# Performance work log

Measured on AMD Instinct MI355X. Metric: run time of the kernel, lower is better.

The kernel has to match this reference:

```python
import jax, jax.numpy as jnp
import numpy as np

B, S, H = 4, 2048, 896
NH, NKV, HD = 14, 2, 64
ROPE_THETA = 1e6


def setup_inputs() -> dict:
    key = jax.random.key(0)
    ks = jax.random.split(key, 8)
    s = 0.02
    return {
        "hidden_states": jax.random.normal(ks[0], (B, S, H), jnp.float32),
        "position_ids": jnp.arange(S, dtype=jnp.int64 if jax.config.jax_enable_x64 else jnp.int32)[None, :],
        "Wq": jax.random.normal(ks[1], (NH * HD, H), jnp.float32) * s,
        "bq": jax.random.normal(ks[2], (NH * HD,), jnp.float32) * s,
        "Wk": jax.random.normal(ks[3], (NKV * HD, H), jnp.float32) * s,
        "bk": jax.random.normal(ks[4], (NKV * HD,), jnp.float32) * s,
        "Wv": jax.random.normal(ks[5], (NKV * HD, H), jnp.float32) * s,
        "bv": jax.random.normal(ks[6], (NKV * HD,), jnp.float32) * s,
        "Wo": jax.random.normal(ks[7], (H, NH * HD), jnp.float32) * s,
    }


def _rope_cos_sin(position_ids, dtype):
    # inv_freq: [HD/2]
    inv_freq = 1.0 / (ROPE_THETA ** (jnp.arange(0, HD, 2, dtype=jnp.float32) / HD))
    # freqs: [1, S, HD/2]
    freqs = position_ids.astype(jnp.float32)[:, :, None] * inv_freq[None, None, :]
    emb = jnp.concatenate([freqs, freqs], axis=-1)  # [1, S, HD]
    return jnp.cos(emb).astype(dtype), jnp.sin(emb).astype(dtype)


def _rotate_half(x):
    x1, x2 = x[..., : HD // 2], x[..., HD // 2 :]
    return jnp.concatenate([-x2, x1], axis=-1)


def reference(hidden_states, position_ids, Wq, bq, Wk, bk, Wv, bv, Wo):
    bsz, q_len, _ = hidden_states.shape
    q = hidden_states @ Wq.T + bq  # [B,S,NH*HD]
    k = hidden_states @ Wk.T + bk  # [B,S,NKV*HD]
    v = hidden_states @ Wv.T + bv
    q = q.reshape(bsz, q_len, NH, HD).transpose(0, 2, 1, 3)    # [B,NH,S,HD]
    k = k.reshape(bsz, q_len, NKV, HD).transpose(0, 2, 1, 3)   # [B,NKV,S,HD]
    v = v.reshape(bsz, q_len, NKV, HD).transpose(0, 2, 1, 3)

    cos, sin = _rope_cos_sin(position_ids, hidden_states.dtype)
    cos, sin = cos[:, None, :, :], sin[:, None, :, :]  # broadcast over heads
    q = q * cos + _rotate_half(q) * sin
    k = k * cos + _rotate_half(k) * sin

    # GQA: repeat kv heads to NH
    n_rep = NH // NKV
    k = jnp.repeat(k, n_rep, axis=1)  # [B,NH,S,HD]
    v = jnp.repeat(v, n_rep, axis=1)

    scale = 1.0 / jnp.sqrt(jnp.asarray(HD, hidden_states.dtype))
    scores = jnp.einsum("bhqd,bhkd->bhqk", q, k) * scale  # [B,NH,S,S]
    causal = jnp.tril(jnp.ones((q_len, q_len), dtype=bool))
    scores = jnp.where(causal[None, None], scores, jnp.finfo(scores.dtype).min)
    probs = jax.nn.softmax(scores, axis=-1)
    attn = jnp.einsum("bhqk,bhkd->bhqd", probs, v)  # [B,NH,S,HD]
    attn = attn.transpose(0, 2, 1, 3).reshape(bsz, q_len, NH * HD)
    return attn @ Wo.T
```

## Files before the change

kernel.cpp:

```cpp
#include <hip/hip_runtime.h>
#include <stdint.h>

#define SB    2048
#define HID   896
#define NHEADS 14
#define NKVH  2
#define HDIM  64
#define BATCH 4
#define MROWS (BATCH*SB)
#define KVW   (NKVH*HDIM)
#define PANEL (SB*HDIM)

typedef short bfrag __attribute__((ext_vector_type(8)));
typedef float f32x4 __attribute__((ext_vector_type(4)));

__device__ __forceinline__ float b2f(unsigned short u) {
    unsigned int x = ((unsigned int)u) << 16;
    float f;
    __builtin_memcpy(&f, &x, 4);
    return f;
}
__device__ __forceinline__ unsigned short f2b(float f) {
    unsigned int x;
    __builtin_memcpy(&x, &f, 4);
    x += 0x7fffu + ((x >> 16) & 1u);
    return (unsigned short)(x >> 16);
}
__device__ __forceinline__ unsigned int pack_bf16(float lo, float hi) {
    unsigned int a, b;
    __builtin_memcpy(&a, &lo, 4);
    __builtin_memcpy(&b, &hi, 4);
    return __builtin_amdgcn_perm(b, a, 0x07060302);
}

__device__ __forceinline__ void async16(void* lds, const void* g) {
    __builtin_amdgcn_global_load_lds(
        (const __attribute__((address_space(1))) unsigned int*)g,
        (__attribute__((address_space(3))) unsigned int*)lds, 16, 0, 0);
}

#define N_HS  (MROWS*HID)
#define N_WQ  (HID*HID)
#define N_BQ  (HID)
#define N_WK  (KVW*HID)
#define N_BK  (KVW)
#define N_WO  (HID*HID)
#define C0 ((size_t)N_HS)
#define C1 (C0 + N_WQ)
#define C2 (C1 + N_BQ)
#define C3 (C2 + N_WK)
#define C4 (C3 + N_BK)
#define C5 (C4 + N_WK)
#define C6 (C5 + N_BK)
#define C7 (C6 + N_WO)

__global__ __launch_bounds__(256) void cvt_kernel(
    const float* __restrict__ a0, const float* __restrict__ a1,
    const float* __restrict__ a2, const float* __restrict__ a3,
    const float* __restrict__ a4, const float* __restrict__ a5,
    const float* __restrict__ a6, const float* __restrict__ a7,
    unsigned short* __restrict__ d0, unsigned short* __restrict__ d1,
    unsigned short* __restrict__ d2, unsigned short* __restrict__ d3,
    unsigned short* __restrict__ d4, unsigned short* __restrict__ d5,
    unsigned short* __restrict__ d6, unsigned short* __restrict__ d7)
{
    size_t i = ((size_t)blockIdx.x * 256 + threadIdx.x) * 4;
    if (i >= C7) return;
    const float* s; unsigned short* d; size_t off;
    if      (i < C0) { s = a0; d = d0; off = i; }
    else if (i < C1) { s = a1; d = d1; off = i - C0; }
    else if (i < C2) { s = a2; d = d2; off = i - C1; }
    else if (i < C3) { s = a3; d = d3; off = i - C2; }
    else if (i < C4) { s = a4; d = d4; off = i - C3; }
    else if (i < C5) { s = a5; d = d5; off = i - C4; }
    else if (i < C6) { s = a6; d = d6; off = i - C5; }
    else             { s = a7; d = d7; off = i - C6; }
    float4 v = *(const float4*)(s + off);
    ushort4 o;
    o.x = f2b(v.x); o.y = f2b(v.y); o.z = f2b(v.z); o.w = f2b(v.w);
    *(ushort4*)(d + off) = o;
}

template<int EPI>
__device__ __forceinline__ void gemm128(
    unsigned short* __restrict__ Al, unsigned short* __restrict__ Bl,
    const unsigned short* __restrict__ A, int lda,
    const unsigned short* __restrict__ W, int ldw,
    const unsigned short* __restrict__ bias,
    void* __restrict__ Cv, int ldc, int m0, int n0, int K,
    unsigned short* __restrict__ VT)
{
    const int tid  = threadIdx.x;
    const int wave = tid >> 6;
    const int lane = tid & 63;
    const int col  = lane & 15;
    const int quad = lane >> 4;
    const int wm   = (wave >> 1) * 64;
    const int wn   = (wave & 1) * 64;
    const int srow = lane >> 2;
    const int scol = (lane & 3) * 8;

    f32x4 acc[4][4] = {};

    auto stage = [&](int buf, int k0) {
#pragma unroll
        for (int i = 0; i < 2; ++i) {
            const int c = wave*2 + i;
            async16(Al + buf*4096 + c*512,
                    A + (size_t)(m0 + c*16 + srow)*lda + k0 + scol);
            async16(Bl + buf*4096 + c*512,
                    W + (size_t)(n0 + c*16 + srow)*ldw + k0 + scol);
        }
    };

    stage(0, 0);
    if (K > 32) stage(1, 32);
    int t = 0;
    for (int k0 = 0; k0 < K; k0 += 32, ++t) {
        const bool more1 = (k0 + 32 < K);
        const bool more2 = (k0 + 64 < K);
        if (more2) stage((t + 2) % 3, k0 + 64);
        if (more2)      asm volatile("s_waitcnt vmcnt(8)" ::: "memory");
        else if (more1) asm volatile("s_waitcnt vmcnt(4)" ::: "memory");
        else            asm volatile("s_waitcnt vmcnt(0)" ::: "memory");
        asm volatile("s_barrier" ::: "memory");
        const unsigned short* Ab = Al + (t % 3)*4096;
        const unsigned short* Bb = Bl + (t % 3)*4096;
        bfrag a[4], b[4];
#pragma unroll
        for (int mb = 0; mb < 4; ++mb)
            a[mb] = *(const bfrag*)(Ab + (wm + mb*16 + col)*32 + quad*8);
#pragma unroll
        for (int nb = 0; nb < 4; ++nb)
            b[nb] = *(const bfrag*)(Bb + (wn + nb*16 + col)*32 + quad*8);
#pragma unroll
        for (int mb = 0; mb < 4; ++mb)
#pragma unroll
            for (int nb = 0; nb < 4; ++nb)
                acc[mb][nb] = __builtin_amdgcn_mfma_f32_16x16x32_bf16(
                    a[mb], b[nb], acc[mb][nb], 0, 0, 0);
        asm volatile("s_barrier" ::: "memory");
    }

    if (EPI == 2) {
#pragma unroll
        for (int nb = 0; nb < 4; ++nb) {
            const int n = wn + nb*16 + col;
            const float bv = b2f(bias[n]);
            const int kvh = n >> 6;
#pragma unroll
            for (int mb = 0; mb < 4; ++mb) {
                const int m = m0 + wm + mb*16 + quad*4;
                const int bb = m >> 11, s = m & (SB-1);
                const int cc = (s >> 5) & 1;
                const int qv = (s >> 3) & 3;
                const int jb = s & 7;
                ushort4 w;
                w.x = f2b(acc[mb][nb][0] + bv);
                w.y = f2b(acc[mb][nb][1] + bv);
                w.z = f2b(acc[mb][nb][2] + bv);
                w.w = f2b(acc[mb][nb][3] + bv);
                *(ushort4*)(VT + (size_t)(bb*NKVH + kvh)*PANEL
                            + (size_t)((s >> 6)*8 + cc*4 + nb)*512
                            + (qv*16 + col)*8 + jb) = w;
            }
        }
    } else {
#pragma unroll
        for (int nb = 0; nb < 4; ++nb) {
            const int n = n0 + wn + nb*16 + col;
            const float bv = bias ? b2f(bias[n]) : 0.0f;
#pragma unroll
            for (int mb = 0; mb < 4; ++mb) {
                const size_t base = (size_t)(m0 + wm + mb*16 + quad*4) * ldc + n;
#pragma unroll
                for (int r = 0; r < 4; ++r) {
                    const float v = acc[mb][nb][r] + bv;
                    if (EPI == 1) ((float*)Cv)[base + (size_t)r * ldc] = v;
                    else ((unsigned short*)Cv)[base + (size_t)r * ldc] = f2b(v);
                }
            }
        }
    }
}

__global__ __launch_bounds__(256) void qkv_gemm(
    const unsigned short* __restrict__ hs,
    const unsigned short* __restrict__ Wq, const unsigned short* __restrict__ bq,
    const unsigned short* __restrict__ Wk, const unsigned short* __restrict__ bk,
    const unsigned short* __restrict__ Wv, const unsigned short* __restrict__ bv,
    unsigned short* __restrict__ Qw, unsigned short* __restrict__ Kw,
    unsigned short* __restrict__ Vp)
{
    __shared__ __align__(16) unsigned short Al[3][128*32];
    __shared__ __align__(16) unsigned short Bl[3][128*32];
    const int m0  = blockIdx.x * 128;
    const int seg = blockIdx.y;
    if (seg < 7)
        gemm128<0>(&Al[0][0], &Bl[0][0], hs, HID, Wq, HID, bq, Qw, HID, m0, seg*128, HID, nullptr);
    else if (seg == 7)
        gemm128<0>(&Al[0][0], &Bl[0][0], hs, HID, Wk, HID, bk, Kw, KVW, m0, 0, HID, nullptr);
    else
        gemm128<2>(&Al[0][0], &Bl[0][0], hs, HID, Wv, HID, bv, nullptr, 0, m0, 0, HID, Vp);
}

__global__ __launch_bounds__(256) void out_gemm(
    const unsigned short* __restrict__ Aw, const unsigned short* __restrict__ Wo,
    float* __restrict__ out)
{
    __shared__ __align__(16) unsigned short Al[3][128*32];
    __shared__ __align__(16) unsigned short Bl[3][128*32];
    gemm128<1>(&Al[0][0], &Bl[0][0], Aw, HID, Wo, HID, nullptr, out, HID,
               blockIdx.x * 128, blockIdx.y * 128, HID, nullptr);
}

__global__ __launch_bounds__(256) void trig_kernel(float2* __restrict__ tab)
{
    const int i = blockIdx.x * 256 + threadIdx.x;
    const int pos = i >> 5, pair = i & 31;
    const float inv = exp2f(-(float)(2*pair) * (19.9315685693f / 64.0f));
    float s, c;
    sincosf((float)pos * inv, &s, &c);
    tab[i] = make_float2(c, s);
}

__global__ __launch_bounds__(256) void rope_kernel(unsigned short* __restrict__ Q,
                                                   const unsigned short* __restrict__ Kw,
                                                   unsigned short* __restrict__ Kp,
                                                   const float2* __restrict__ tab)
{
    const int idx  = blockIdx.x * 256 + threadIdx.x;
    const int pair = idx & 31;
    const int head = (idx >> 5) & 15;
    const int m    = idx >> 9;
    const int pos  = m & (SB - 1);
    const float2 cs = tab[pos*32 + pair];
    const float c = cs.x, s = cs.y;
    if (head < NHEADS) {
        const float mul = 0.1803368801111f;
        unsigned short* base = Q + (size_t)m * HID + (size_t)head * HDIM;
        const float x1 = b2f(base[pair]);
        const float x2 = b2f(base[pair + 32]);
        base[pair]      = f2b((x1 * c - x2 * s) * mul);
        base[pair + 32] = f2b((x2 * c + x1 * s) * mul);
    } else {
        const int kvh = head - NHEADS;
        const unsigned short* src = Kw + (size_t)m * KVW + (size_t)kvh * HDIM;
        const float x1 = b2f(src[pair]);
        const float x2 = b2f(src[pair + 32]);
        const float y1 = x1 * c - x2 * s;
        const float y2 = x2 * c + x1 * s;
        const int bb = m >> 11, sq = m & (SB - 1);
        const int tile = sq >> 6, r6 = sq & 63;
        const int kb = r6 >> 4, colk = r6 & 15;
        const int quad = pair >> 3, j = pair & 7;
        unsigned short* panel = Kp + (size_t)(bb*NKVH + kvh) * PANEL;
        const size_t off0 = (size_t)(tile*8 + kb*2)*512 + (quad*16 + colk)*8 + j;
        panel[off0]       = f2b(y1);
        panel[off0 + 512] = f2b(y2);
    }
}

__global__ __launch_bounds__(64, 2) void flash_kernel(
    const unsigned short* __restrict__ Q,
    const unsigned short* __restrict__ Kp,
    const unsigned short* __restrict__ Vp,
    unsigned short* __restrict__ Aw)
{
    const int bid  = blockIdx.x;
    const int cidx = bid / 56;
    const int hb   = bid - cidx * 56;
    const int h    = hb % NHEADS;
    const int b    = hb / NHEADS;
    const int kvh  = h / 7;
    const int chunk = 63 - cidx;

    const int lane = threadIdx.x;
    const int col  = lane & 15;
    const int quad = lane >> 4;

    const int idxA = (col + ((quad & 1) << 5)) << 2;
    const int idxB = idxA + 64;
    const bool hi  = (quad >= 2);

    const unsigned short* Qb  = Q  + (size_t)b * SB * HID + (size_t)h * HDIM;
    const unsigned short* Kpp = Kp + (size_t)(b*NKVH + kvh) * PANEL;
    const unsigned short* Vpp = Vp + (size_t)(b*NKVH + kvh) * PANEL;

    bfrag ones;
#pragma unroll
    for (int jj = 0; jj < 8; ++jj) ones[jj] = (short)0x3F80;

    const int qrow  = chunk * 32;
    const int nsteps = (chunk >> 1) + 1;

    bfrag qf[2][2];
#pragma unroll
    for (int qb = 0; qb < 2; ++qb) {
        const unsigned short* qr = Qb + (size_t)(qrow + qb*16 + col) * HID;
        qf[qb][0] = *(const bfrag*)(qr + quad*8);
        qf[qb][1] = *(const bfrag*)(qr + 32 + quad*8);
    }

    f32x4 o[2][4] = {};
    f32x4 lac[2] = {};

    f32x4 scur[2][4];
    {
        bfrag kc0[4][2];
#pragma unroll
        for (int kb = 0; kb < 4; ++kb) {
            kc0[kb][0] = *(const bfrag*)(Kpp + (size_t)(kb*2 + 0)*512 + lane*8);
            kc0[kb][1] = *(const bfrag*)(Kpp + (size_t)(kb*2 + 1)*512 + lane*8);
        }
#pragma unroll
        for (int kb = 0; kb < 4; ++kb)
#pragma unroll
            for (int qb = 0; qb < 2; ++qb) {
                f32x4 z = {};
                z = __builtin_amdgcn_mfma_f32_16x16x32_bf16(kc0[kb][0], qf[qb][0], z, 0, 0, 0);
                z = __builtin_amdgcn_mfma_f32_16x16x32_bf16(kc0[kb][1], qf[qb][1], z, 0, 0, 0);
                scur[qb][kb] = z;
            }
    }

    for (int step = 0; step < nsteps; ++step) {
        const size_t T = (size_t)step * 4096;
        const bool more = (step + 1 < nsteps);

        bfrag vf[2][4];
#pragma unroll
        for (int cc = 0; cc < 2; ++cc)
#pragma unroll
            for (int nb = 0; nb < 4; ++nb)
                vf[cc][nb] = *(const bfrag*)(Vpp + T + (cc*4 + nb)*512 + lane*8);
        bfrag kn[4][2];
        if (more) {
#pragma unroll
            for (int kb = 0; kb < 4; ++kb) {
                kn[kb][0] = *(const bfrag*)(Kpp + T + 4096 + (kb*2+0)*512 + lane*8);
                kn[kb][1] = *(const bfrag*)(Kpp + T + 4096 + (kb*2+1)*512 + lane*8);
            }
        }

        const int k0 = step * 64;
        unsigned int pk[2][4][2];
#pragma unroll
        for (int qb = 0; qb < 2; ++qb) {
            float pv[4][4];
#pragma unroll
            for (int kb = 0; kb < 4; ++kb)
#pragma unroll
                for (int r = 0; r < 4; ++r)
                    pv[kb][r] = __builtin_amdgcn_exp2f(scur[qb][kb][r]);
            if (step == nsteps - 1) {
                const int q = qrow + qb*16 + col;
#pragma unroll
                for (int kb = 0; kb < 4; ++kb)
#pragma unroll
                    for (int r = 0; r < 4; ++r)
                        if (k0 + kb*16 + quad*4 + r > q) pv[kb][r] = 0.f;
            }
#pragma unroll
            for (int kb = 0; kb < 4; ++kb) {
                pk[qb][kb][0] = pack_bf16(pv[kb][0], pv[kb][1]);
                pk[qb][kb][1] = pack_bf16(pv[kb][2], pv[kb][3]);
            }
        }

#pragma unroll
        for (int cc = 0; cc < 2; ++cc)
#pragma unroll
            for (int qb = 0; qb < 2; ++qb) {
                unsigned int D[4];
#pragma unroll
                for (int jj = 0; jj < 4; ++jj) {
                    const int idx = (jj < 2) ? idxA : idxB;
                    const int t0 = __builtin_amdgcn_ds_bpermute(idx, (int)pk[qb][2*cc][jj & 1]);
                    const int t1 = __builtin_amdgcn_ds_bpermute(idx, (int)pk[qb][2*cc+1][jj & 1]);
                    D[jj] = (unsigned int)(hi ? t1 : t0);
                }
                bfrag pf;
                __builtin_memcpy(&pf, D, 16);
                lac[qb] = __builtin_amdgcn_mfma_f32_16x16x32_bf16(ones, pf, lac[qb], 0, 0, 0);
#pragma unroll
                for (int nb = 0; nb < 4; ++nb)
                    o[qb][nb] = __builtin_amdgcn_mfma_f32_16x16x32_bf16(
                        vf[cc][nb], pf, o[qb][nb], 0, 0, 0);
            }

        if (more) {
            f32x4 snext[2][4];
#pragma unroll
            for (int kb = 0; kb < 4; ++kb)
#pragma unroll
                for (int qb = 0; qb < 2; ++qb) {
                    f32x4 z = {};
                    z = __builtin_amdgcn_mfma_f32_16x16x32_bf16(kn[kb][0], qf[qb][0], z, 0, 0, 0);
                    z = __builtin_amdgcn_mfma_f32_16x16x32_bf16(kn[kb][1], qf[qb][1], z, 0, 0, 0);
                    snext[qb][kb] = z;
                }
#pragma unroll
            for (int qb = 0; qb < 2; ++qb)
#pragma unroll
                for (int kb = 0; kb < 4; ++kb)
                    scur[qb][kb] = snext[qb][kb];
        }
    }

#pragma unroll
    for (int qb = 0; qb < 2; ++qb) {
        const float inv = 1.0f / lac[qb][0];
        const size_t row = (size_t)b * SB + qrow + qb*16 + col;
#pragma unroll
        for (int nb = 0; nb < 4; ++nb) {
            ushort4 w;
            w.x = f2b(o[qb][nb][0] * inv);
            w.y = f2b(o[qb][nb][1] * inv);
            w.z = f2b(o[qb][nb][2] * inv);
            w.w = f2b(o[qb][nb][3] * inv);
            *(ushort4*)(Aw + row * HID + h*HDIM + nb*16 + quad*4) = w;
        }
    }
}

extern "C" void kernel_launch(void* const* d_in, const int* in_sizes, int n_in,
                              void* d_out, int out_size, void* d_ws, size_t ws_size,
                              hipStream_t stream)
{
    (void)in_sizes; (void)n_in; (void)out_size; (void)ws_size;
    const float* hs_f = (const float*)d_in[0];
    const float* Wq_f = (const float*)d_in[2];
    const float* bq_f = (const float*)d_in[3];
    const float* Wk_f = (const float*)d_in[4];
    const float* bk_f = (const float*)d_in[5];
    const float* Wv_f = (const float*)d_in[6];
    const float* bv_f = (const float*)d_in[7];
    const float* Wo_f = (const float*)d_in[8];
    float* out = (float*)d_out;

    char* ws = (char*)d_ws;
    float2* tab = (float2*)ws;
    ws += ((size_t)SB * 32 * sizeof(float2) + 255) & ~(size_t)255;
    auto take = [&](size_t elems) {
        unsigned short* p = (unsigned short*)ws;
        ws += ((elems * 2 + 255) & ~(size_t)255);
        return p;
    };
    unsigned short* hs = take(N_HS);
    unsigned short* Wq = take(N_WQ);
    unsigned short* bq = take(N_BQ);
    unsigned short* Wk = take(N_WK);
    unsigned short* bk = take(N_BK);
    unsigned short* Wv = take(N_WK);
    unsigned short* bv = take(N_BK);
    unsigned short* Wo = take(N_WO);
    unsigned short* Qw = take((size_t)MROWS * HID);
    unsigned short* Kw = take((size_t)MROWS * KVW);
    unsigned short* Kp = take((size_t)MROWS * KVW);
    unsigned short* Vp = take((size_t)MROWS * KVW);
    unsigned short* Aw = take((size_t)MROWS * HID);

    trig_kernel<<<dim3(SB*32/256), 256, 0, stream>>>(tab);
    cvt_kernel<<<dim3((C7/4 + 255)/256), 256, 0, stream>>>(
        hs_f, Wq_f, bq_f, Wk_f, bk_f, Wv_f, bv_f, Wo_f,
        hs, Wq, bq, Wk, bk, Wv, bv, Wo);
    qkv_gemm<<<dim3(MROWS/128, 9), 256, 0, stream>>>(hs, Wq, bq, Wk, bk, Wv, bv,
                                                     Qw, Kw, Vp);
    rope_kernel<<<dim3((MROWS*16*32)/256), 256, 0, stream>>>(Qw, Kw, Kp, tab);
    flash_kernel<<<dim3(64*NHEADS*BATCH), 64, 0, stream>>>(Qw, Kp, Vp, Aw);
    out_gemm<<<dim3(MROWS/128, HID/128), 256, 0, stream>>>(Aw, Wo, out);
}
```

Baseline: 197.8 us.

## Fuse RoPE into QKV GEMM epilogue and merge trig table into convert kernel

Applies rotary embedding and the Q scale directly in the QKV GEMM epilogue, pairing accumulator blocks nb and nb+2 so each wave holds both halves of a head. K is rotated and written straight into the flash panel layout, which removes the separate rope kernel and the Kw intermediate buffer round trip. The cos/sin table is now built by extra blocks appended to the convert kernel, saving a launch. The cost is scattered table loads and uncoalesced 2-byte stores in the epilogue.

```diff
diff --git a/kernel.cpp b/kernel.cpp
--- a/kernel.cpp
+++ b/kernel.cpp
@@ -10,6 +10,7 @@
 #define MROWS (BATCH*SB)
 #define KVW   (NKVH*HDIM)
 #define PANEL (SB*HDIM)
+#define QSC   0.1803368801111f
 
 typedef short bfrag __attribute__((ext_vector_type(8)));
 typedef float f32x4 __attribute__((ext_vector_type(4)));
@@ -53,6 +54,7 @@
 #define C5 (C4 + N_WK)
 #define C6 (C5 + N_BK)
 #define C7 (C6 + N_WO)
+#define NB_CVT ((C7/4 + 255)/256)
 
 __global__ __launch_bounds__(256) void cvt_kernel(
     const float* __restrict__ a0, const float* __restrict__ a1,
@@ -62,8 +64,18 @@
     unsigned short* __restrict__ d0, unsigned short* __restrict__ d1,
     unsigned short* __restrict__ d2, unsigned short* __restrict__ d3,
     unsigned short* __restrict__ d4, unsigned short* __restrict__ d5,
-    unsigned short* __restrict__ d6, unsigned short* __restrict__ d7)
-{
+    unsigned short* __restrict__ d6, unsigned short* __restrict__ d7,
+    float2* __restrict__ tab)
+{
+    if (blockIdx.x >= NB_CVT) {
+        const int i = (blockIdx.x - (int)NB_CVT) * 256 + threadIdx.x;
+        const int pos = i >> 5, pair = i & 31;
+        const float inv = exp2f(-(float)(2*pair) * (19.9315685693f / 64.0f));
+        float s, c;
+        sincosf((float)pos * inv, &s, &c);
+        tab[i] = make_float2(c, s);
+        return;
+    }
     size_t i = ((size_t)blockIdx.x * 256 + threadIdx.x) * 4;
     if (i >= C7) return;
     const float* s; unsigned short* d; size_t off;
@@ -88,7 +100,7 @@
     const unsigned short* __restrict__ W, int ldw,
     const unsigned short* __restrict__ bias,
     void* __restrict__ Cv, int ldc, int m0, int n0, int K,
-    unsigned short* __restrict__ VT)
+    unsigned short* __restrict__ VT, const float2* __restrict__ tab)
 {
     const int tid  = threadIdx.x;
     const int wave = tid >> 6;
@@ -165,6 +177,59 @@
                             + (qv*16 + col)*8 + jb) = w;
             }
         }
+    } else if (EPI == 3) {
+#pragma unroll
+        for (int nb = 0; nb < 2; ++nb) {
+            const int n  = n0 + wn + nb*16 + col;
+            const float bv0 = b2f(bias[n]);
+            const float bv2 = b2f(bias[n + 32]);
+            const int pair = nb*16 + col;
+#pragma unroll
+            for (int mb = 0; mb < 4; ++mb) {
+                const int row = m0 + wm + mb*16 + quad*4;
+                const size_t base = (size_t)row * ldc;
+#pragma unroll
+                for (int r = 0; r < 4; ++r) {
+                    const int pos = (row + r) & (SB-1);
+                    const float2 cs = tab[pos*32 + pair];
+                    const float xl = acc[mb][nb][r]   + bv0;
+                    const float xh = acc[mb][nb+2][r] + bv2;
+                    ((unsigned short*)Cv)[base + (size_t)r*ldc + n]
+                        = f2b((xl*cs.x - xh*cs.y) * QSC);
+                    ((unsigned short*)Cv)[base + (size_t)r*ldc + n + 32]
+                        = f2b((xh*cs.x + xl*cs.y) * QSC);
+                }
+            }
+        }
+    } else if (EPI == 4) {
+#pragma unroll
+        for (int nb = 0; nb < 2; ++nb) {
+            const int n   = wn + nb*16 + col;
+            const int kvh = n >> 6;
+            const int pair = n & 63;
+            const float bv0 = b2f(bias[n]);
+            const float bv2 = b2f(bias[n + 32]);
+            const int dq = pair >> 3, j = pair & 7;
+#pragma unroll
+            for (int mb = 0; mb < 4; ++mb) {
+                const int m = m0 + wm + mb*16 + quad*4;
+                const int bb = m >> 11;
+                unsigned short* pan = VT + (size_t)(bb*NKVH + kvh)*PANEL;
+#pragma unroll
+                for (int r = 0; r < 4; ++r) {
+                    const int s = (m + r) & (SB-1);
+                    const float2 cs = tab[s*32 + pair];
+                    const float xl = acc[mb][nb][r]   + bv0;
+                    const float xh = acc[mb][nb+2][r] + bv2;
+                    const int tile = s >> 6, sk = s & 63;
+                    const int kb = sk >> 4, colk = sk & 15;
+                    const size_t off = (size_t)(tile*8 + kb*2)*512
+                                     + (dq*16 + colk)*8 + j;
+                    pan[off]       = f2b(xl*cs.x - xh*cs.y);
+                    pan[off + 512] = f2b(xh*cs.x + xl*cs.y);
+                }
+            }
+        }
     } else {
 #pragma unroll
         for (int nb = 0; nb < 4; ++nb) {
@@ -176,8 +241,7 @@
 #pragma unroll
                 for (int r = 0; r < 4; ++r) {
                     const float v = acc[mb][nb][r] + bv;
-                    if (EPI == 1) ((float*)Cv)[base + (size_t)r * ldc] = v;
-                    else ((unsigned short*)Cv)[base + (size_t)r * ldc] = f2b(v);
+                    ((float*)Cv)[base + (size_t)r * ldc] = v;
                 }
             }
         }
@@ -189,19 +253,22 @@
     const unsigned short* __restrict__ Wq, const unsigned short* __restrict__ bq,
     const unsigned short* __restrict__ Wk, const unsigned short* __restrict__ bk,
     const unsigned short* __restrict__ Wv, const unsigned short* __restrict__ bv,
-    unsigned short* __restrict__ Qw, unsigned short* __restrict__ Kw,
-    unsigned short* __restrict__ Vp)
+    unsigned short* __restrict__ Qw, unsigned short* __restrict__ Kp,
+    unsigned short* __restrict__ Vp, const float2* __restrict__ tab)
 {
     __shared__ __align__(16) unsigned short Al[3][128*32];
     __shared__ __align__(16) unsigned short Bl[3][128*32];
     const int m0  = blockIdx.x * 128;
     const int seg = blockIdx.y;
     if (seg < 7)
-        gemm128<0>(&Al[0][0], &Bl[0][0], hs, HID, Wq, HID, bq, Qw, HID, m0, seg*128, HID, nullptr);
+        gemm128<3>(&Al[0][0], &Bl[0][0], hs, HID, Wq, HID, bq, Qw, HID,
+                   m0, seg*128, HID, nullptr, tab);
     else if (seg == 7)
-        gemm128<0>(&Al[0][0], &Bl[0][0], hs, HID, Wk, HID, bk, Kw, KVW, m0, 0, HID, nullptr);
+        gemm128<4>(&Al[0][0], &Bl[0][0], hs, HID, Wk, HID, bk, nullptr, 0,
+                   m0, 0, HID, Kp, tab);
     else
-        gemm128<2>(&Al[0][0], &Bl[0][0], hs, HID, Wv, HID, bv, nullptr, 0, m0, 0, HID, Vp);
+        gemm128<2>(&Al[0][0], &Bl[0][0], hs, HID, Wv, HID, bv, nullptr, 0,
+                   m0, 0, HID, Vp, nullptr);
 }
 
 __global__ __launch_bounds__(256) void out_gemm(
@@ -211,54 +278,7 @@
     __shared__ __align__(16) unsigned short Al[3][128*32];
     __shared__ __align__(16) unsigned short Bl[3][128*32];
     gemm128<1>(&Al[0][0], &Bl[0][0], Aw, HID, Wo, HID, nullptr, out, HID,
-               blockIdx.x * 128, blockIdx.y * 128, HID, nullptr);
-}
-
-__global__ __launch_bounds__(256) void trig_kernel(float2* __restrict__ tab)
-{
-    const int i = blockIdx.x * 256 + threadIdx.x;
-    const int pos = i >> 5, pair = i & 31;
-    const float inv = exp2f(-(float)(2*pair) * (19.9315685693f / 64.0f));
-    float s, c;
-    sincosf((float)pos * inv, &s, &c);
-    tab[i] = make_float2(c, s);
-}
-
-__global__ __launch_bounds__(256) void rope_kernel(unsigned short* __restrict__ Q,
-                                                   const unsigned short* __restrict__ Kw,
-                                                   unsigned short* __restrict__ Kp,
-                                                   const float2* __restrict__ tab)
-{
-    const int idx  = blockIdx.x * 256 + threadIdx.x;
-    const int pair = idx & 31;
-    const int head = (idx >> 5) & 15;
-    const int m    = idx >> 9;
-    const int pos  = m & (SB - 1);
-    const float2 cs = tab[pos*32 + pair];
-    const float c = cs.x, s = cs.y;
-    if (head < NHEADS) {
-        const float mul = 0.1803368801111f;
-        unsigned short* base = Q + (size_t)m * HID + (size_t)head * HDIM;
-        const float x1 = b2f(base[pair]);
-        const float x2 = b2f(base[pair + 32]);
-        base[pair]      = f2b((x1 * c - x2 * s) * mul);
-        base[pair + 32] = f2b((x2 * c + x1 * s) * mul);
-    } else {
-        const int kvh = head - NHEADS;
-        const unsigned short* src = Kw + (size_t)m * KVW + (size_t)kvh * HDIM;
-        const float x1 = b2f(src[pair]);
-        const float x2 = b2f(src[pair + 32]);
-        const float y1 = x1 * c - x2 * s;
-        const float y2 = x2 * c + x1 * s;
-        const int bb = m >> 11, sq = m & (SB - 1);
-        const int tile = sq >> 6, r6 = sq & 63;
-        const int kb = r6 >> 4, colk = r6 & 15;
-        const int quad = pair >> 3, j = pair & 7;
-        unsigned short* panel = Kp + (size_t)(bb*NKVH + kvh) * PANEL;
-        const size_t off0 = (size_t)(tile*8 + kb*2)*512 + (quad*16 + colk)*8 + j;
-        panel[off0]       = f2b(y1);
-        panel[off0 + 512] = f2b(y2);
-    }
+               blockIdx.x * 128, blockIdx.y * 128, HID, nullptr, nullptr);
 }
 
 __global__ __launch_bounds__(64, 2) void flash_kernel(
@@ -456,18 +476,15 @@
     unsigned short* bv = take(N_BK);
     unsigned short* Wo = take(N_WO);
     unsigned short* Qw = take((size_t)MROWS * HID);
-    unsigned short* Kw = take((size_t)MROWS * KVW);
     unsigned short* Kp = take((size_t)MROWS * KVW);
     unsigned short* Vp = take((size_t)MROWS * KVW);
     unsigned short* Aw = take((size_t)MROWS * HID);
 
-    trig_kernel<<<dim3(SB*32/256), 256, 0, stream>>>(tab);
-    cvt_kernel<<<dim3((C7/4 + 255)/256), 256, 0, stream>>>(
+    cvt_kernel<<<dim3(NB_CVT + 256), 256, 0, stream>>>(
         hs_f, Wq_f, bq_f, Wk_f, bk_f, Wv_f, bv_f, Wo_f,
-        hs, Wq, bq, Wk, bk, Wv, bv, Wo);
+        hs, Wq, bq, Wk, bk, Wv, bv, Wo, tab);
     qkv_gemm<<<dim3(MROWS/128, 9), 256, 0, stream>>>(hs, Wq, bq, Wk, bk, Wv, bv,
-                                                     Qw, Kw, Vp);
-    rope_kernel<<<dim3((MROWS*16*32)/256), 256, 0, stream>>>(Qw, Kw, Kp, tab);
+                                                     Qw, Kp, Vp, tab);
     flash_kernel<<<dim3(64*NHEADS*BATCH), 64, 0, stream>>>(Qw, Kp, Vp, Aw);
     out_gemm<<<dim3(MROWS/128, HID/128), 256, 0, stream>>>(Aw, Wo, out);
 }
```

Measured after the change: 191.8 us. 3.1% less time.
